# Performance work log

Hardware: AMD Instinct MI355X
Metric: run time of the kernel (lower is better)

Reference implementation:

```python
import jax, jax.numpy as jnp
import numpy as np


def setup_inputs() -> dict:
    key = jax.random.key(0)
    k1, k2, k3, k4 = jax.random.split(key, 4)
    n, m = 4096, 1024  # n video frames, 1024-d features
    scale = 0.02
    return {
        "x": jax.random.normal(k1, (n, m), dtype=jnp.float32),
        "WQ": jax.random.normal(k2, (m, m), dtype=jnp.float32) * scale,  # torch Linear weight [out,in]
        "WK": jax.random.normal(k3, (m, m), dtype=jnp.float32) * scale,
        "WV": jax.random.normal(k4, (m, m), dtype=jnp.float32) * scale,
    }


def _quaternion_logits(q, k):
    """Hamilton-product attention logits: 4 tensors of shape [Lq, Lk]."""
    qr, qx, qy, qz = jnp.split(q, 4, axis=-1)
    kr, kx, ky, kz = jnp.split(k, 4, axis=-1)
    dot = lambda a, b: jnp.einsum('qd,kd->qk', a, b)
    r = dot(qr, kr) - dot(qx, kx) - dot(qy, ky) - dot(qz, kz)
    i = dot(qr, kx) + dot(qx, kr) + dot(qy, kz) - dot(qz, ky)
    j = dot(qr, ky) - dot(qx, kz) + dot(qy, kr) + dot(qz, kx)
    kk = dot(qr, kz) + dot(qx, ky) - dot(qy, kx) + dot(qz, kr)
    return [r, i, j, kk]


def reference(x, WQ, WK, WV):
    # QKV projections (torch Linear, no bias): y = x @ W.T
    Q = x @ WQ.T
    K = x @ WK.T
    V = x @ WV.T
    v_vals = jnp.split(V, 4, axis=-1)  # 4 chunks of depth d/4 (tensor2tensor quaternion attn)
    logits = _quaternion_logits(Q, K)
    outs = []
    w = None
    for l, v in zip(logits, v_vals):
        w = jax.nn.softmax(l, axis=-1)  # per-component softmax over keys
        outs.append(w @ v)
    y = jnp.concatenate(outs, axis=-1)  # [n, d]
    # original returns the attention weights from the last component (loop-leaked var)
    return y, w
```

## Files before the change

kernel.cpp:

```cpp
#include <hip/hip_runtime.h>
#include <cmath>

typedef __attribute__((ext_vector_type(8))) short short8;
typedef __attribute__((ext_vector_type(8))) _Float16 half8;
typedef __attribute__((ext_vector_type(4))) float f32x4;
typedef unsigned short u16;

__device__ __forceinline__ u16 f2h(float f) {
    _Float16 h = (_Float16)f;
    return __builtin_bit_cast(u16, h);
}
__device__ __forceinline__ float h2f(u16 b) {
    return (float)__builtin_bit_cast(_Float16, b);
}

#define GLD16(g, l)                                                              \
    __builtin_amdgcn_global_load_lds(                                            \
        (const __attribute__((address_space(1))) unsigned int*)(g),              \
        (__attribute__((address_space(3))) unsigned int*)(l), 16, 0, 0)

#define MFMA_F16(a, b, c)                                                        \
    __builtin_amdgcn_mfma_f32_16x16x32_f16(                                      \
        __builtin_bit_cast(half8, (a)), __builtin_bit_cast(half8, (b)), (c), 0, 0, 0)
#define SBAR() asm volatile("s_barrier" ::: "memory")

__global__ __launch_bounds__(256) void to_h(const float* __restrict__ in,
                                            u16* __restrict__ out) {
    int idx = blockIdx.x * 256 + threadIdx.x;
    float4 v = reinterpret_cast<const float4*>(in)[idx];
    ushort4 h;
    h.x = f2h(v.x); h.y = f2h(v.y); h.z = f2h(v.z); h.w = f2h(v.w);
    reinterpret_cast<ushort4*>(out)[idx] = h;
}

__global__ __launch_bounds__(512, 2) void logits8(
    const u16* __restrict__ A, const u16* __restrict__ B, const u16* __restrict__ Bneg,
    float* __restrict__ C, float* __restrict__ pm, float* __restrict__ ps,
    int perm_packed, int sign_packed)
{
    constexpr int NT = 16;
    __shared__ u16 L[2][2][256 * 64];
    const int tid = threadIdx.x;
    const int l = tid & 63, w = tid >> 6;
    const int wr = w >> 2, wc = w & 3;
    const int lr = l & 15, lh = l >> 4;
    const int bid = (int)blockIdx.x;
    const int swz = (bid & 7) * 32 + (bid >> 3);
    const int row0 = (swz >> 4) * 256, col0 = (swz & 15) * 256;
    const int tc = col0 >> 8;
    const int srow = l >> 3;
    const int scol = ((l & 7) ^ (l >> 3)) * 8;

    f32x4 acc[8][4] = {};

    auto stage = [&](int t) {
        int kA = t * 64;
        int ch = kA >> 8;
        int p = (perm_packed >> (2 * ch)) & 3;
        const u16* Bsrc = ((sign_packed >> ch) & 1) ? Bneg : B;
        int kB = (p << 8) + (kA & 255);
        int bf = t & 1;
        #pragma unroll
        for (int i = 0; i < 4; ++i) {
            int r0 = w * 32 + i * 8;
            GLD16(&A[(size_t)(row0 + r0 + srow) * 1024 + kA + scol], &L[bf][0][r0 * 64]);
        }
        #pragma unroll
        for (int i = 0; i < 4; ++i) {
            int r0 = w * 32 + i * 8;
            GLD16(&Bsrc[(size_t)(col0 + r0 + srow) * 1024 + kB + scol], &L[bf][1][r0 * 64]);
        }
    };
    auto readA = [&](int bf, int m, int kh) -> short8 {
        int row = wr * 128 + m * 16 + lr;
        int c = ((kh * 4 + lh) ^ (lr & 7)) * 8;
        return *reinterpret_cast<const short8*>(&L[bf][0][row * 64 + c]);
    };
    auto readB = [&](int bf, int n, int kh) -> short8 {
        int row = wc * 64 + n * 16 + lr;
        int c = ((kh * 4 + lh) ^ (lr & 7)) * 8;
        return *reinterpret_cast<const short8*>(&L[bf][1][row * 64 + c]);
    };

    stage(0);
    stage(1);
    asm volatile("s_waitcnt vmcnt(8)" ::: "memory");
    SBAR();

    #pragma unroll 2
    for (int t = 0; t < NT; ++t) {
        const int bf = t & 1;
        short8 am[4][2], bn[4][2];
        #pragma unroll
        for (int m = 0; m < 4; ++m) { am[m][0] = readA(bf, m, 0); am[m][1] = readA(bf, m, 1); }
        #pragma unroll
        for (int n = 0; n < 2; ++n) { bn[n][0] = readB(bf, n, 0); bn[n][1] = readB(bf, n, 1); }
        SBAR();
        __builtin_amdgcn_s_setprio(1);
        #pragma unroll
        for (int m = 0; m < 4; ++m)
            #pragma unroll
            for (int n = 0; n < 2; ++n) {
                acc[m][n] = MFMA_F16(am[m][0], bn[n][0], acc[m][n]);
                acc[m][n] = MFMA_F16(am[m][1], bn[n][1], acc[m][n]);
            }
        __builtin_amdgcn_s_setprio(0);
        SBAR();
        #pragma unroll
        for (int n = 2; n < 4; ++n) { bn[n][0] = readB(bf, n, 0); bn[n][1] = readB(bf, n, 1); }
        SBAR();
        __builtin_amdgcn_s_setprio(1);
        #pragma unroll
        for (int m = 0; m < 4; ++m)
            #pragma unroll
            for (int n = 2; n < 4; ++n) {
                acc[m][n] = MFMA_F16(am[m][0], bn[n][0], acc[m][n]);
                acc[m][n] = MFMA_F16(am[m][1], bn[n][1], acc[m][n]);
            }
        __builtin_amdgcn_s_setprio(0);
        SBAR();
        #pragma unroll
        for (int m = 0; m < 4; ++m) { am[m][0] = readA(bf, 4 + m, 0); am[m][1] = readA(bf, 4 + m, 1); }
        SBAR();
        __builtin_amdgcn_s_setprio(1);
        #pragma unroll
        for (int m = 0; m < 4; ++m)
            #pragma unroll
            for (int n = 2; n < 4; ++n) {
                acc[4 + m][n] = MFMA_F16(am[m][0], bn[n][0], acc[4 + m][n]);
                acc[4 + m][n] = MFMA_F16(am[m][1], bn[n][1], acc[4 + m][n]);
            }
        __builtin_amdgcn_s_setprio(0);
        SBAR();
        if (t + 2 < NT) stage(t + 2);
        SBAR();
        __builtin_amdgcn_s_setprio(1);
        #pragma unroll
        for (int m = 0; m < 4; ++m)
            #pragma unroll
            for (int n = 0; n < 2; ++n) {
                acc[4 + m][n] = MFMA_F16(am[m][0], bn[n][0], acc[4 + m][n]);
                acc[4 + m][n] = MFMA_F16(am[m][1], bn[n][1], acc[4 + m][n]);
            }
        __builtin_amdgcn_s_setprio(0);
        if (t + 2 < NT) { asm volatile("s_waitcnt vmcnt(8)" ::: "memory"); }
        else           { asm volatile("s_waitcnt vmcnt(0)" ::: "memory"); }
        SBAR();
    }

    float* sc  = reinterpret_cast<float*>(&L[0][0][0]);
    float* sc2 = sc + 1024;
    __syncthreads();
    #pragma unroll
    for (int m = 0; m < 8; ++m)
        #pragma unroll
        for (int j = 0; j < 4; ++j) {
            float v = fmaxf(fmaxf(acc[m][0][j], acc[m][1][j]),
                            fmaxf(acc[m][2][j], acc[m][3][j]));
            #pragma unroll
            for (int off = 1; off < 16; off <<= 1) v = fmaxf(v, __shfl_xor(v, off, 16));
            if (lr == 0) sc[(wr * 128 + m * 16 + lh * 4 + j) * 4 + wc] = v;
        }
    __syncthreads();
    #pragma unroll
    for (int m = 0; m < 8; ++m)
        #pragma unroll
        for (int j = 0; j < 4; ++j) {
            int row = wr * 128 + m * 16 + lh * 4 + j;
            float M = fmaxf(fmaxf(sc[row * 4 + 0], sc[row * 4 + 1]),
                            fmaxf(sc[row * 4 + 2], sc[row * 4 + 3]));
            float s = expf(acc[m][0][j] - M) + expf(acc[m][1][j] - M)
                    + expf(acc[m][2][j] - M) + expf(acc[m][3][j] - M);
            #pragma unroll
            for (int off = 1; off < 16; off <<= 1) s += __shfl_xor(s, off, 16);
            if (lr == 0) sc2[row * 4 + wc] = s;
        }
    __syncthreads();
    if (wc == 0 && lr == 0) {
        #pragma unroll
        for (int m = 0; m < 8; ++m)
            #pragma unroll
            for (int j = 0; j < 4; ++j) {
                int row = wr * 128 + m * 16 + lh * 4 + j;
                float M = fmaxf(fmaxf(sc[row * 4 + 0], sc[row * 4 + 1]),
                                fmaxf(sc[row * 4 + 2], sc[row * 4 + 3]));
                float S = sc2[row * 4 + 0] + sc2[row * 4 + 1]
                        + sc2[row * 4 + 2] + sc2[row * 4 + 3];
                pm[(size_t)(row0 + row) * 16 + tc] = M;
                ps[(size_t)(row0 + row) * 16 + tc] = S;
            }
    }

    #pragma unroll
    for (int m = 0; m < 8; ++m)
        #pragma unroll
        for (int n = 0; n < 4; ++n) {
            int gr = row0 + wr * 128 + m * 16 + lh * 4;
            int gc = col0 + wc * 64 + n * 16 + lr;
            #pragma unroll
            for (int j = 0; j < 4; ++j)
                C[(size_t)(gr + j) * 4096 + gc] = acc[m][n][j];
        }
}

__global__ __launch_bounds__(512, 2) void qkv8(
    const u16* __restrict__ A, const u16* __restrict__ B,
    u16* __restrict__ Qh, u16* __restrict__ Kh, u16* __restrict__ Khn,
    u16* __restrict__ Vt)
{
    constexpr int NT = 16;
    __shared__ u16 L[2][2][256 * 64];
    const int tid = threadIdx.x;
    const int l = tid & 63, w = tid >> 6;
    const int wr = w >> 2, wc = w & 3;
    const int lr = l & 15, lh = l >> 4;
    const int bid = (int)blockIdx.x;
    const int wgid = (bid & 7) * 24 + (bid >> 3);
    const int row0 = (wgid / 12) * 256, col0 = (wgid % 12) * 256;
    const int srow = l >> 3;
    const int scol = ((l & 7) ^ (l >> 3)) * 8;

    f32x4 acc[8][4] = {};

    auto stage = [&](int t) {
        int k0 = t * 64;
        int bf = t & 1;
        #pragma unroll
        for (int i = 0; i < 4; ++i) {
            int r0 = w * 32 + i * 8;
            GLD16(&A[(size_t)(row0 + r0 + srow) * 1024 + k0 + scol], &L[bf][0][r0 * 64]);
        }
        #pragma unroll
        for (int i = 0; i < 4; ++i) {
            int r0 = w * 32 + i * 8;
            GLD16(&B[(size_t)(col0 + r0 + srow) * 1024 + k0 + scol], &L[bf][1][r0 * 64]);
        }
    };
    auto readA = [&](int bf, int m, int kh) -> short8 {
        int row = wr * 128 + m * 16 + lr;
        int c = ((kh * 4 + lh) ^ (lr & 7)) * 8;
        return *reinterpret_cast<const short8*>(&L[bf][0][row * 64 + c]);
    };
    auto readB = [&](int bf, int n, int kh) -> short8 {
        int row = wc * 64 + n * 16 + lr;
        int c = ((kh * 4 + lh) ^ (lr & 7)) * 8;
        return *reinterpret_cast<const short8*>(&L[bf][1][row * 64 + c]);
    };

    stage(0);
    stage(1);
    asm volatile("s_waitcnt vmcnt(8)" ::: "memory");
    SBAR();

    #pragma unroll 2
    for (int t = 0; t < NT; ++t) {
        const int bf = t & 1;
        short8 am[4][2], bn[4][2];
        #pragma unroll
        for (int m = 0; m < 4; ++m) { am[m][0] = readA(bf, m, 0); am[m][1] = readA(bf, m, 1); }
        #pragma unroll
        for (int n = 0; n < 2; ++n) { bn[n][0] = readB(bf, n, 0); bn[n][1] = readB(bf, n, 1); }
        SBAR();
        __builtin_amdgcn_s_setprio(1);
        #pragma unroll
        for (int m = 0; m < 4; ++m)
            #pragma unroll
            for (int n = 0; n < 2; ++n) {
                acc[m][n] = MFMA_F16(am[m][0], bn[n][0], acc[m][n]);
                acc[m][n] = MFMA_F16(am[m][1], bn[n][1], acc[m][n]);
            }
        __builtin_amdgcn_s_setprio(0);
        SBAR();
        #pragma unroll
        for (int n = 2; n < 4; ++n) { bn[n][0] = readB(bf, n, 0); bn[n][1] = readB(bf, n, 1); }
        SBAR();
        __builtin_amdgcn_s_setprio(1);
        #pragma unroll
        for (int m = 0; m < 4; ++m)
            #pragma unroll
            for (int n = 2; n < 4; ++n) {
                acc[m][n] = MFMA_F16(am[m][0], bn[n][0], acc[m][n]);
                acc[m][n] = MFMA_F16(am[m][1], bn[n][1], acc[m][n]);
            }
        __builtin_amdgcn_s_setprio(0);
        SBAR();
        #pragma unroll
        for (int m = 0; m < 4; ++m) { am[m][0] = readA(bf, 4 + m, 0); am[m][1] = readA(bf, 4 + m, 1); }
        SBAR();
        __builtin_amdgcn_s_setprio(1);
        #pragma unroll
        for (int m = 0; m < 4; ++m)
            #pragma unroll
            for (int n = 2; n < 4; ++n) {
                acc[4 + m][n] = MFMA_F16(am[m][0], bn[n][0], acc[4 + m][n]);
                acc[4 + m][n] = MFMA_F16(am[m][1], bn[n][1], acc[4 + m][n]);
            }
        __builtin_amdgcn_s_setprio(0);
        SBAR();
        if (t + 2 < NT) stage(t + 2);
        SBAR();
        __builtin_amdgcn_s_setprio(1);
        #pragma unroll
        for (int m = 0; m < 4; ++m)
            #pragma unroll
            for (int n = 0; n < 2; ++n) {
                acc[4 + m][n] = MFMA_F16(am[m][0], bn[n][0], acc[4 + m][n]);
                acc[4 + m][n] = MFMA_F16(am[m][1], bn[n][1], acc[4 + m][n]);
            }
        __builtin_amdgcn_s_setprio(0);
        if (t + 2 < NT) { asm volatile("s_waitcnt vmcnt(8)" ::: "memory"); }
        else           { asm volatile("s_waitcnt vmcnt(0)" ::: "memory"); }
        SBAR();
    }

    const int mode = col0 >> 10;
    #pragma unroll
    for (int m = 0; m < 8; ++m)
        #pragma unroll
        for (int n = 0; n < 4; ++n) {
            int gr = row0 + wr * 128 + m * 16 + lh * 4;
            int gc = col0 + wc * 64 + n * 16 + lr;
            int gcl = gc & 1023;
            f32x4 v = acc[m][n];
            if (mode == 0) {
                #pragma unroll
                for (int j = 0; j < 4; ++j)
                    Qh[(size_t)(gr + j) * 1024 + gcl] = f2h(v[j]);
            } else if (mode == 1) {
                #pragma unroll
                for (int j = 0; j < 4; ++j) {
                    u16 h = f2h(v[j]);
                    size_t o = (size_t)(gr + j) * 1024 + gcl;
                    Kh[o] = h; Khn[o] = h ^ 0x8000;
                }
            } else {
                ushort4 o;
                o.x = f2h(v[0]); o.y = f2h(v[1]); o.z = f2h(v[2]); o.w = f2h(v[3]);
                *reinterpret_cast<ushort4*>(&Vt[(size_t)gcl * 4096 + gr]) = o;
            }
        }
}

template<bool WRITE_W>
__global__ __launch_bounds__(256) void pv_fused(
    const float* __restrict__ Lw, float* __restrict__ Wout,
    const u16* __restrict__ Vt, const float* __restrict__ pm,
    const float* __restrict__ ps, u16* __restrict__ ypart, int c256)
{
    __shared__ u16 As[64 * 64];
    __shared__ u16 Bs[256 * 64];
    __shared__ float Ms[64], Is[64];
    const int tid = threadIdx.x;
    const int l = tid & 63, w = tid >> 6;
    const int lr = l & 15, lh = l >> 4;
    const int kc = blockIdx.x;
    const int row0 = blockIdx.y * 64;
    const int kbase = kc * 512;
    const int srow = l >> 3, scol = ((l & 7) ^ (l >> 3)) * 8;

    if (tid < 64) {
        const float* pmr = &pm[(size_t)(row0 + tid) * 16];
        const float* psr = &ps[(size_t)(row0 + tid) * 16];
        float M = -INFINITY;
        #pragma unroll
        for (int i = 0; i < 16; ++i) M = fmaxf(M, pmr[i]);
        float S = 0.f;
        #pragma unroll
        for (int i = 0; i < 16; ++i) S += psr[i] * expf(pmr[i] - M);
        Ms[tid] = M; Is[tid] = 1.0f / S;
    }
    __syncthreads();

    float Mr[4], Ir[4];
    #pragma unroll
    for (int i = 0; i < 4; ++i) { int r = (tid >> 4) + i * 16; Mr[i] = Ms[r]; Ir[i] = Is[r]; }

    f32x4 acc[4][4] = {};

    for (int kt = 0; kt < 8; ++kt) {
        __syncthreads();
        #pragma unroll
        for (int i = 0; i < 4; ++i) {
            int idx = tid + i * 256;
            int r = idx >> 4, s4 = idx & 15;
            size_t ga = (size_t)(row0 + r) * 4096 + kbase + kt * 64 + s4 * 4;
            float4 v = *reinterpret_cast<const float4*>(&Lw[ga]);
            float e0 = expf(v.x - Mr[i]) * Ir[i];
            float e1 = expf(v.y - Mr[i]) * Ir[i];
            float e2 = expf(v.z - Mr[i]) * Ir[i];
            float e3 = expf(v.w - Mr[i]) * Ir[i];
            if (WRITE_W)
                *reinterpret_cast<float4*>(&Wout[ga]) = make_float4(e0, e1, e2, e3);
            ushort4 h;
            h.x = f2h(e0); h.y = f2h(e1); h.z = f2h(e2); h.w = f2h(e3);
            int dst = ((s4 >> 1) ^ (r & 7)) * 8 + (s4 & 1) * 4;
            *reinterpret_cast<ushort4*>(&As[r * 64 + dst]) = h;
        }
        #pragma unroll
        for (int i = 0; i < 8; ++i) {
            int r0 = w * 64 + i * 8;
            GLD16(&Vt[(size_t)(c256 + r0 + srow) * 4096 + kbase + kt * 64 + scol],
                  &Bs[r0 * 64]);
        }
        __syncthreads();
        #pragma unroll
        for (int kh = 0; kh < 2; ++kh) {
            short8 af[4], bfv[4];
            #pragma unroll
            for (int m = 0; m < 4; ++m)
                af[m] = *reinterpret_cast<const short8*>(
                    &As[(m * 16 + lr) * 64 + ((kh * 4 + lh) ^ (lr & 7)) * 8]);
            #pragma unroll
            for (int n = 0; n < 4; ++n)
                bfv[n] = *reinterpret_cast<const short8*>(
                    &Bs[(w * 64 + n * 16 + lr) * 64 + ((kh * 4 + lh) ^ (lr & 7)) * 8]);
            #pragma unroll
            for (int m = 0; m < 4; ++m)
                #pragma unroll
                for (int n = 0; n < 4; ++n)
                    acc[m][n] = MFMA_F16(af[m], bfv[n], acc[m][n]);
        }
    }

    #pragma unroll
    for (int m = 0; m < 4; ++m)
        #pragma unroll
        for (int n = 0; n < 4; ++n) {
            int rr = m * 16 + lh * 4;
            int col = w * 64 + n * 16 + lr;
            #pragma unroll
            for (int j = 0; j < 4; ++j)
                ypart[((size_t)kc * 4096 + row0 + rr + j) * 256 + col] = f2h(acc[m][n][j]);
        }
}

__global__ __launch_bounds__(256) void reduce_y(const u16* __restrict__ ypart,
                                                float* __restrict__ y, int c256)
{
    int idx = blockIdx.x * 256 + threadIdx.x;
    int r = idx >> 6, c4 = (idx & 63) * 4;
    float s0 = 0.f, s1 = 0.f, s2 = 0.f, s3 = 0.f;
    #pragma unroll
    for (int kc = 0; kc < 8; ++kc) {
        ushort4 p = *reinterpret_cast<const ushort4*>(
            &ypart[((size_t)kc * 4096 + r) * 256 + c4]);
        s0 += h2f(p.x); s1 += h2f(p.y); s2 += h2f(p.z); s3 += h2f(p.w);
    }
    *reinterpret_cast<float4*>(&y[(size_t)r * 1024 + c256 + c4]) =
        make_float4(s0, s1, s2, s3);
}

extern "C" void kernel_launch(void* const* d_in, const int* in_sizes, int n_in,
                              void* d_out, int out_size, void* d_ws, size_t ws_size,
                              hipStream_t stream)
{
    const int n = 4096, d = 1024;
    const float* x  = (const float*)d_in[0];
    const float* WQ = (const float*)d_in[1];
    const float* WK = (const float*)d_in[2];
    const float* WV = (const float*)d_in[3];

    float* y = (float*)d_out;
    float* w = y + (size_t)n * d;

    u16* xh   = (u16*)d_ws;
    u16* Wh   = xh  + (size_t)n * 1024;
    u16* Qh   = Wh  + (size_t)3 * d * 1024;
    u16* Kh   = Qh  + (size_t)n * 1024;
    u16* Khn  = Kh  + (size_t)n * 1024;
    u16* Vt   = Khn + (size_t)n * 1024;
    u16* ypart = Vt + (size_t)d * 4096;
    float* pm = (float*)(ypart + (size_t)8 * n * 256);
    float* ps = pm + (size_t)n * 16;

    to_h<<<n * d / 1024, 256, 0, stream>>>(x, xh);
    to_h<<<d * d / 1024, 256, 0, stream>>>(WQ, Wh);
    to_h<<<d * d / 1024, 256, 0, stream>>>(WK, Wh + (size_t)d * 1024);
    to_h<<<d * d / 1024, 256, 0, stream>>>(WV, Wh + (size_t)2 * d * 1024);

    qkv8<<<192, 512, 0, stream>>>(xh, Wh, Qh, Kh, Khn, Vt);

    const int permv[4] = {0xE4, 0xB1, 0x4E, 0x1B};
    const int signv[4] = {0x0E, 0x08, 0x02, 0x04};

    for (int c = 0; c < 4; ++c) {
        logits8<<<256, 512, 0, stream>>>(Qh, Kh, Khn, w, pm, ps, permv[c], signv[c]);
        if (c == 3)
            pv_fused<true><<<dim3(8, 64), 256, 0, stream>>>(w, w, Vt, pm, ps, ypart, c * 256);
        else
            pv_fused<false><<<dim3(8, 64), 256, 0, stream>>>(w, w, Vt, pm, ps, ypart, c * 256);
        reduce_y<<<1024, 256, 0, stream>>>(ypart, y, c * 256);
    }
}
```

Baseline: 405.5 us.

## Store logits as fp16 offsets from per-wave max and drop block-level softmax reduction

The logits kernel now writes each logit as an fp16 value relative to a per-wave 64-column max, and writes per-64-column max/sum partials straight from registers. This removes the LDS round-trips and syncthreads in its epilogue and halves logit traffic to and from global memory. The PV kernel reads the fp16 deltas, adds a per-tile offset correction, and merges 64 partials per row with a 4-way cooperative reduction. The logits buffer reuses workspace that also holds xh and Wh, which are dead by then. Accuracy risk: fp16 storage of logit deltas loses precision in the softmax weights that are returned.

```diff
diff --git a/kernel.cpp b/kernel.cpp
--- a/kernel.cpp
+++ b/kernel.cpp
@@ -35,7 +35,7 @@
 
 __global__ __launch_bounds__(512, 2) void logits8(
     const u16* __restrict__ A, const u16* __restrict__ B, const u16* __restrict__ Bneg,
-    float* __restrict__ C, float* __restrict__ pm, float* __restrict__ ps,
+    u16* __restrict__ Ch, float* __restrict__ pm, float* __restrict__ ps,
     int perm_packed, int sign_packed)
 {
     constexpr int NT = 16;
@@ -47,7 +47,6 @@
     const int bid = (int)blockIdx.x;
     const int swz = (bid & 7) * 32 + (bid >> 3);
     const int row0 = (swz >> 4) * 256, col0 = (swz & 15) * 256;
-    const int tc = col0 >> 8;
     const int srow = l >> 3;
     const int scol = ((l & 7) ^ (l >> 3)) * 8;
 
@@ -148,59 +147,31 @@
         SBAR();
     }
 
-    float* sc  = reinterpret_cast<float*>(&L[0][0][0]);
-    float* sc2 = sc + 1024;
-    __syncthreads();
+    const int tcol = (col0 >> 6) + wc;
     #pragma unroll
-    for (int m = 0; m < 8; ++m)
+    for (int m = 0; m < 8; ++m) {
         #pragma unroll
         for (int j = 0; j < 4; ++j) {
+            int row = row0 + wr * 128 + m * 16 + lh * 4 + j;
             float v = fmaxf(fmaxf(acc[m][0][j], acc[m][1][j]),
                             fmaxf(acc[m][2][j], acc[m][3][j]));
             #pragma unroll
             for (int off = 1; off < 16; off <<= 1) v = fmaxf(v, __shfl_xor(v, off, 16));
-            if (lr == 0) sc[(wr * 128 + m * 16 + lh * 4 + j) * 4 + wc] = v;
-        }
-    __syncthreads();
-    #pragma unroll
-    for (int m = 0; m < 8; ++m)
-        #pragma unroll
-        for (int j = 0; j < 4; ++j) {
-            int row = wr * 128 + m * 16 + lh * 4 + j;
-            float M = fmaxf(fmaxf(sc[row * 4 + 0], sc[row * 4 + 1]),
-                            fmaxf(sc[row * 4 + 2], sc[row * 4 + 3]));
-            float s = expf(acc[m][0][j] - M) + expf(acc[m][1][j] - M)
-                    + expf(acc[m][2][j] - M) + expf(acc[m][3][j] - M);
+            float s = expf(acc[m][0][j] - v) + expf(acc[m][1][j] - v)
+                    + expf(acc[m][2][j] - v) + expf(acc[m][3][j] - v);
             #pragma unroll
             for (int off = 1; off < 16; off <<= 1) s += __shfl_xor(s, off, 16);
-            if (lr == 0) sc2[row * 4 + wc] = s;
-        }
-    __syncthreads();
-    if (wc == 0 && lr == 0) {
-        #pragma unroll
-        for (int m = 0; m < 8; ++m)
-            #pragma unroll
-            for (int j = 0; j < 4; ++j) {
-                int row = wr * 128 + m * 16 + lh * 4 + j;
-                float M = fmaxf(fmaxf(sc[row * 4 + 0], sc[row * 4 + 1]),
-                                fmaxf(sc[row * 4 + 2], sc[row * 4 + 3]));
-                float S = sc2[row * 4 + 0] + sc2[row * 4 + 1]
-                        + sc2[row * 4 + 2] + sc2[row * 4 + 3];
-                pm[(size_t)(row0 + row) * 16 + tc] = M;
-                ps[(size_t)(row0 + row) * 16 + tc] = S;
-            }
-    }
-
-    #pragma unroll
-    for (int m = 0; m < 8; ++m)
-        #pragma unroll
-        for (int n = 0; n < 4; ++n) {
-            int gr = row0 + wr * 128 + m * 16 + lh * 4;
-            int gc = col0 + wc * 64 + n * 16 + lr;
-            #pragma unroll
-            for (int j = 0; j < 4; ++j)
-                C[(size_t)(gr + j) * 4096 + gc] = acc[m][n][j];
-        }
+            if (lr == 0) {
+                pm[(size_t)row * 64 + tcol] = v;
+                ps[(size_t)row * 64 + tcol] = s;
+            }
+            #pragma unroll
+            for (int n = 0; n < 4; ++n) {
+                int gc = col0 + wc * 64 + n * 16 + lr;
+                Ch[(size_t)row * 4096 + gc] = f2h(acc[m][n][j] - v);
+            }
+        }
+    }
 }
 
 __global__ __launch_bounds__(512, 2) void qkv8(
@@ -343,12 +314,13 @@
 
 template<bool WRITE_W>
 __global__ __launch_bounds__(256) void pv_fused(
-    const float* __restrict__ Lw, float* __restrict__ Wout,
+    const u16* __restrict__ Lh, float* __restrict__ Wout,
     const u16* __restrict__ Vt, const float* __restrict__ pm,
     const float* __restrict__ ps, u16* __restrict__ ypart, int c256)
 {
     __shared__ u16 As[64 * 64];
     __shared__ u16 Bs[256 * 64];
+    __shared__ float Red[64][4];
     __shared__ float Ms[64], Is[64];
     const int tid = threadIdx.x;
     const int l = tid & 63, w = tid >> 6;
@@ -358,18 +330,30 @@
     const int kbase = kc * 512;
     const int srow = l >> 3, scol = ((l & 7) ^ (l >> 3)) * 8;
 
-    if (tid < 64) {
-        const float* pmr = &pm[(size_t)(row0 + tid) * 16];
-        const float* psr = &ps[(size_t)(row0 + tid) * 16];
+    {
+        int row = tid & 63, part = tid >> 6;
+        const float* pmr = &pm[(size_t)(row0 + row) * 64 + part * 16];
+        const float* psr = &ps[(size_t)(row0 + row) * 64 + part * 16];
         float M = -INFINITY;
         #pragma unroll
         for (int i = 0; i < 16; ++i) M = fmaxf(M, pmr[i]);
+        Red[row][part] = M;
+        __syncthreads();
+        float Mg = fmaxf(fmaxf(Red[row][0], Red[row][1]),
+                         fmaxf(Red[row][2], Red[row][3]));
         float S = 0.f;
         #pragma unroll
-        for (int i = 0; i < 16; ++i) S += psr[i] * expf(pmr[i] - M);
-        Ms[tid] = M; Is[tid] = 1.0f / S;
-    }
-    __syncthreads();
+        for (int i = 0; i < 16; ++i) S += psr[i] * expf(pmr[i] - Mg);
+        __syncthreads();
+        Red[row][part] = S;
+        __syncthreads();
+        if (tid < 64) {
+            float Sg = Red[tid][0] + Red[tid][1] + Red[tid][2] + Red[tid][3];
+            Ms[tid] = Mg;
+            Is[tid] = 1.0f / Sg;
+        }
+        __syncthreads();
+    }
 
     float Mr[4], Ir[4];
     #pragma unroll
@@ -378,17 +362,19 @@
     f32x4 acc[4][4] = {};
 
     for (int kt = 0; kt < 8; ++kt) {
+        const int tcol = kc * 8 + kt;
         __syncthreads();
         #pragma unroll
         for (int i = 0; i < 4; ++i) {
             int idx = tid + i * 256;
             int r = idx >> 4, s4 = idx & 15;
+            float coff = pm[(size_t)(row0 + r) * 64 + tcol] - Mr[i];
             size_t ga = (size_t)(row0 + r) * 4096 + kbase + kt * 64 + s4 * 4;
-            float4 v = *reinterpret_cast<const float4*>(&Lw[ga]);
-            float e0 = expf(v.x - Mr[i]) * Ir[i];
-            float e1 = expf(v.y - Mr[i]) * Ir[i];
-            float e2 = expf(v.z - Mr[i]) * Ir[i];
-            float e3 = expf(v.w - Mr[i]) * Ir[i];
+            ushort4 dv = *reinterpret_cast<const ushort4*>(&Lh[ga]);
+            float e0 = expf(h2f(dv.x) + coff) * Ir[i];
+            float e1 = expf(h2f(dv.y) + coff) * Ir[i];
+            float e2 = expf(h2f(dv.z) + coff) * Ir[i];
+            float e3 = expf(h2f(dv.w) + coff) * Ir[i];
             if (WRITE_W)
                 *reinterpret_cast<float4*>(&Wout[ga]) = make_float4(e0, e1, e2, e3);
             ushort4 h;
@@ -461,17 +447,18 @@
     const float* WV = (const float*)d_in[3];
 
     float* y = (float*)d_out;
-    float* w = y + (size_t)n * d;
-
-    u16* xh   = (u16*)d_ws;
-    u16* Wh   = xh  + (size_t)n * 1024;
-    u16* Qh   = Wh  + (size_t)3 * d * 1024;
+    float* wout = y + (size_t)n * d;
+
+    u16* Lh   = (u16*)d_ws;
+    u16* xh   = Lh;
+    u16* Wh   = Lh + (size_t)n * 1024;
+    u16* Qh   = Lh + (size_t)n * 4096;
     u16* Kh   = Qh  + (size_t)n * 1024;
     u16* Khn  = Kh  + (size_t)n * 1024;
     u16* Vt   = Khn + (size_t)n * 1024;
     u16* ypart = Vt + (size_t)d * 4096;
     float* pm = (float*)(ypart + (size_t)8 * n * 256);
-    float* ps = pm + (size_t)n * 16;
+    float* ps = pm + (size_t)n * 64;
 
     to_h<<<n * d / 1024, 256, 0, stream>>>(x, xh);
     to_h<<<d * d / 1024, 256, 0, stream>>>(WQ, Wh);
@@ -484,11 +471,11 @@
     const int signv[4] = {0x0E, 0x08, 0x02, 0x04};
 
     for (int c = 0; c < 4; ++c) {
-        logits8<<<256, 512, 0, stream>>>(Qh, Kh, Khn, w, pm, ps, permv[c], signv[c]);
+        logits8<<<256, 512, 0, stream>>>(Qh, Kh, Khn, Lh, pm, ps, permv[c], signv[c]);
         if (c == 3)
-            pv_fused<true><<<dim3(8, 64), 256, 0, stream>>>(w, w, Vt, pm, ps, ypart, c * 256);
+            pv_fused<true><<<dim3(8, 64), 256, 0, stream>>>(Lh, wout, Vt, pm, ps, ypart, c * 256);
         else
-            pv_fused<false><<<dim3(8, 64), 256, 0, stream>>>(w, w, Vt, pm, ps, ypart, c * 256);
+            pv_fused<false><<<dim3(8, 64), 256, 0, stream>>>(Lh, wout, Vt, pm, ps, ypart, c * 256);
         reduce_y<<<1024, 256, 0, stream>>>(ypart, y, c * 256);
     }
 }
```

Result: faster. 374.3 us (-7.7%).
